# Kernel optimization log

Hardware: AMD Instinct MI355X
Metric: run time of the kernel (lower is better)

## Reference

```python
import jax, jax.numpy as jnp
import numpy as np

B, S, E, H = 4, 1024, 1024, 16
D = E // H  # head_dim = 64


def _rope_tables(seq_len, dim, base=10000.0):
    inv = 1.0 / (base ** (np.arange(0, dim, 2, dtype=np.float32) / dim))
    t = np.arange(seq_len, dtype=np.float32)
    freqs = np.outer(t, inv)                      # (S, D/2)
    emb = np.concatenate([freqs, freqs], axis=-1)  # (S, D)
    return (jnp.asarray(np.cos(emb))[None, None],  # (1,1,S,D)
            jnp.asarray(np.sin(emb))[None, None])


def setup_inputs() -> dict:
    key = jax.random.key(0)
    ks = jax.random.split(key, 12)
    std = 1.0 / np.sqrt(E)
    cos, sin = _rope_tables(S, D)
    # causal additive mask (2D, broadcast inside reference)
    neg = jnp.finfo(jnp.float32).min
    causal = jnp.where(jnp.tril(jnp.ones((S, S), dtype=bool)), 0.0, neg).astype(jnp.float32)
    return {
        "query": jax.random.normal(ks[0], (B, S, E), jnp.float32),
        "key": jax.random.normal(ks[1], (B, S, E), jnp.float32),
        "value": jax.random.normal(ks[2], (B, S, E), jnp.float32),
        "cos": cos,
        "sin": sin,
        "attn_mask": causal,
        "Wq": jax.random.uniform(ks[3], (E, E), jnp.float32, -std, std),
        "bq": jax.random.uniform(ks[4], (E,), jnp.float32, -std, std),
        "Wk": jax.random.uniform(ks[5], (E, E), jnp.float32, -std, std),
        "bk": jax.random.uniform(ks[6], (E,), jnp.float32, -std, std),
        "Wv": jax.random.uniform(ks[7], (E, E), jnp.float32, -std, std),
        "bv": jax.random.uniform(ks[8], (E,), jnp.float32, -std, std),
        "Wo": jax.random.uniform(ks[9], (E, E), jnp.float32, -std, std),
        "bo": jax.random.uniform(ks[10], (E,), jnp.float32, -std, std),
    }


def _rotate_half(x):
    x1, x2 = jnp.split(x, 2, axis=-1)
    return jnp.concatenate([-x2, x1], axis=-1)


def reference(query, key, value, cos, sin, attn_mask, Wq, bq, Wk, bk, Wv, bv, Wo, bo):
    b, sq, e = query.shape
    sk = key.shape[1]
    scale = D ** -0.5
    # projections (Linear stored as (in, out))
    q = (query @ Wq + bq).reshape(b, sq, H, D).transpose(0, 2, 1, 3)  # (B,H,Sq,D)
    k = (key @ Wk + bk).reshape(b, sk, H, D).transpose(0, 2, 1, 3)    # (B,H,Sk,D)
    v = (value @ Wv + bv).reshape(b, sk, H, D).transpose(0, 2, 1, 3)
    # rotary position embedding
    q = q * cos + _rotate_half(q) * sin
    k = k * cos + _rotate_half(k) * sin
    # scaled dot-product attention with additive mask
    scores = jnp.einsum("bhqd,bhkd->bhqk", q, k) * scale
    scores = scores + attn_mask[None, None]  # 2D mask -> broadcast over batch, heads
    attn = jax.nn.softmax(scores, axis=-1)
    out = jnp.einsum("bhqk,bhkd->bhqd", attn, v)
    out = out.transpose(0, 2, 1, 3).reshape(b, sq, e)
    return out @ Wo + bo
```

## Files before the change

kernel.cpp:

```cpp
#include <hip/hip_runtime.h>
#include <cmath>

#define S_LEN 1024
#define E_DIM 1024
#define NHEAD 16
#define HDIM  64
#define NBATCH 4
#define MROWS (NBATCH * S_LEN)

typedef unsigned short u16;
typedef unsigned long long u64;
typedef __bf16 bf16x8 __attribute__((ext_vector_type(8)));
typedef float  f32x4  __attribute__((ext_vector_type(4)));
typedef float  f4     __attribute__((ext_vector_type(4)));

union U64x2 { u64 u[2]; bf16x8 v; };

__device__ __forceinline__ float bf2f(u16 u) {
    union { unsigned int i; float f; } v; v.i = ((unsigned int)u) << 16; return v.f;
}
__device__ __forceinline__ u16 f2bf(float f) {
    union { float f; unsigned int i; } v; v.f = f;
    return (u16)((v.i + 0x7fffu + ((v.i >> 16) & 1u)) >> 16);
}
__device__ __forceinline__ int probe_f32(const void* cosT) {
    return ((const u16*)cosT)[0] != 0x3F80;
}
__device__ __forceinline__ void load16(u16* dst, const void* src, size_t eidx, int f32) {
    if (!f32) {
        const u16* p = (const u16*)src + eidx;
        *reinterpret_cast<int4*>(dst)     = *reinterpret_cast<const int4*>(p);
        *reinterpret_cast<int4*>(dst + 8) = *reinterpret_cast<const int4*>(p + 8);
    } else {
        const f4* p = reinterpret_cast<const f4*>((const float*)src + eidx);
        f4 a = p[0], b = p[1], c = p[2], d = p[3];
        dst[0]=f2bf(a.x);  dst[1]=f2bf(a.y);  dst[2]=f2bf(a.z);  dst[3]=f2bf(a.w);
        dst[4]=f2bf(b.x);  dst[5]=f2bf(b.y);  dst[6]=f2bf(b.z);  dst[7]=f2bf(b.w);
        dst[8]=f2bf(c.x);  dst[9]=f2bf(c.y);  dst[10]=f2bf(c.z); dst[11]=f2bf(c.w);
        dst[12]=f2bf(d.x); dst[13]=f2bf(d.y); dst[14]=f2bf(d.z); dst[15]=f2bf(d.w);
    }
}
__device__ __forceinline__ float ld1(const void* p, size_t i, int f32) {
    return f32 ? ((const float*)p)[i] : bf2f(((const u16*)p)[i]);
}
__device__ __forceinline__ void st1(void* p, size_t i, float v, int f32) {
    if (f32) ((float*)p)[i] = v; else ((u16*)p)[i] = f2bf(v);
}
__device__ __forceinline__ void gload16(const u16* gp, u16* lbase) {
    __builtin_amdgcn_global_load_lds(
        (const __attribute__((address_space(1))) void*)gp,
        (__attribute__((address_space(3))) void*)lbase, 16, 0, 0);
}

__global__ __launch_bounds__(256) void transpose_w(
    const void* __restrict__ W0, const void* __restrict__ W1,
    const void* __restrict__ W2, const void* __restrict__ W3,
    u16* __restrict__ T0, u16* __restrict__ T1,
    u16* __restrict__ T2, u16* __restrict__ T3,
    const void* __restrict__ cosT)
{
    __shared__ __align__(16) u16 tile[64][72];
    const int f32 = probe_f32(cosT);
    const int z = blockIdx.z;
    const void* W = (z == 0) ? W0 : (z == 1) ? W1 : (z == 2) ? W2 : W3;
    u16* T        = (z == 0) ? T0 : (z == 1) ? T1 : (z == 2) ? T2 : T3;
    const int r0 = blockIdx.y * 64, c0 = blockIdx.x * 64;
    const int tr = threadIdx.x >> 2, tc = (threadIdx.x & 3) * 16;

    load16(&tile[tr][tc], W, (size_t)(r0 + tr) * 1024 + c0 + tc, f32);
    __syncthreads();

    u16 buf[16];
#pragma unroll
    for (int j = 0; j < 16; ++j) buf[j] = tile[tc + j][tr];
    u16* dst = T + (size_t)(c0 + tr) * 1024 + r0 + tc;
    *reinterpret_cast<int4*>(dst)     = *reinterpret_cast<int4*>(buf);
    *reinterpret_cast<int4*>(dst + 8) = *reinterpret_cast<int4*>(buf + 8);
}

__device__ __forceinline__ void gemm_body64(
    const void* __restrict__ A, int aF, const u16* __restrict__ Wt,
    const void* __restrict__ bias, const void* __restrict__ cosT,
    const void* __restrict__ sinT, int tblF, void* __restrict__ C, int cF,
    int rope, float oscale, int m0, int n0)
{
    __shared__ __align__(16) u16 As[2][64 * 32];
    __shared__ __align__(16) u16 Bs[2][128 * 32];

    const int tid = threadIdx.x;
    const int w = tid >> 6, lane = tid & 63;
    const int lhi = lane >> 4, llo = lane & 15;
    const int jb0 = 4 * (w >> 1) + (w & 1);

    f32x4 acc[4][2];
#pragma unroll
    for (int i = 0; i < 4; ++i)
#pragma unroll
        for (int j = 0; j < 2; ++j) acc[i][j] = (f32x4){0.f, 0.f, 0.f, 0.f};

    const int srow = lane >> 2, spos = lane & 3;

    auto stage = [&](int buf, int k0) {
        if (!aF) {
            const int rowA = 16 * w + srow;
            const int cA = spos ^ ((rowA >> 1) & 3);
            gload16((const u16*)A + (size_t)(m0 + rowA) * 1024 + k0 + 8 * cA,
                    &As[buf][w * 512]);
        } else if (tid < 128) {
            const int row = tid >> 1, hc = tid & 1;
            u16 tmp[16];
            load16(tmp, A, (size_t)(m0 + row) * 1024 + k0 + 16 * hc, aF);
            const int g = (row >> 1) & 3;
            *reinterpret_cast<int4*>(&As[buf][row * 32 + ((2 * hc) ^ g) * 8]) =
                *reinterpret_cast<int4*>(tmp);
            *reinterpret_cast<int4*>(&As[buf][row * 32 + ((2 * hc + 1) ^ g) * 8]) =
                *reinterpret_cast<int4*>(tmp + 8);
        }
#pragma unroll
        for (int ss = 0; ss < 2; ++ss) {
            const int s = w + 4 * ss;
            const int row = 16 * s + srow;
            const int c = spos ^ ((row >> 1) & 3);
            gload16(Wt + (size_t)(n0 + row) * 1024 + k0 + 8 * c, &Bs[buf][s * 512]);
        }
    };

    auto compute = [&](int buf) {
        bf16x8 af[4], bfr[2];
#pragma unroll
        for (int mb = 0; mb < 4; ++mb) {
            const int r = 16 * mb + llo;
            af[mb] = *reinterpret_cast<const bf16x8*>(
                &As[buf][r * 32 + 8 * (lhi ^ ((r >> 1) & 3))]);
        }
#pragma unroll
        for (int j = 0; j < 2; ++j) {
            const int r = 16 * (jb0 + 2 * j) + llo;
            bfr[j] = *reinterpret_cast<const bf16x8*>(
                &Bs[buf][r * 32 + 8 * (lhi ^ ((r >> 1) & 3))]);
        }
#pragma unroll
        for (int mb = 0; mb < 4; ++mb)
#pragma unroll
            for (int j = 0; j < 2; ++j)
                acc[mb][j] = __builtin_amdgcn_mfma_f32_16x16x32_bf16(
                    af[mb], bfr[j], acc[mb][j], 0, 0, 0);
    };

    stage(0, 0);
    __syncthreads();
    int cur = 0;
    for (int k0 = 0; k0 < 1024; k0 += 32) {
        if (k0 + 32 < 1024) stage(cur ^ 1, k0 + 32);
        compute(cur);
        __syncthreads();
        cur ^= 1;
    }

    if (!rope) {
#pragma unroll
        for (int j = 0; j < 2; ++j) {
            const int colw = n0 + 16 * (jb0 + 2 * j) + llo;
            float bv = ld1(bias, colw, tblF);
#pragma unroll
            for (int mb = 0; mb < 4; ++mb) {
                int row = m0 + 16 * mb + 4 * lhi;
#pragma unroll
                for (int i = 0; i < 4; ++i)
                    st1(C, (size_t)(row + i) * 1024 + colw, acc[mb][j][i] + bv, cF);
            }
        }
    } else {
        const int d1 = 16 * (w & 1) + llo;
        const int c1 = n0 + 64 * (w >> 1) + d1;
        float b1 = ld1(bias, c1, tblF);
        float b2 = ld1(bias, c1 + 32, tblF);
#pragma unroll
        for (int mb = 0; mb < 4; ++mb) {
            int row = m0 + 16 * mb + 4 * lhi;
#pragma unroll
            for (int i = 0; i < 4; ++i) {
                int s = (row + i) & (S_LEN - 1);
                float c  = ld1(cosT, s * HDIM + d1, tblF);
                float sn = ld1(sinT, s * HDIM + d1, tblF);
                float x1 = acc[mb][0][i] + b1;
                float x2 = acc[mb][1][i] + b2;
                st1(C, (size_t)(row + i) * 1024 + c1,      (x1 * c - x2 * sn) * oscale, cF);
                st1(C, (size_t)(row + i) * 1024 + c1 + 32, (x2 * c + x1 * sn) * oscale, cF);
            }
        }
    }
}

__device__ __forceinline__ void gemm_body32(
    const void* __restrict__ A, int aF, const u16* __restrict__ Wt,
    const void* __restrict__ bias, const void* __restrict__ cosT,
    const void* __restrict__ sinT, int tblF, void* __restrict__ C, int cF,
    int rope, float oscale, int m0, int n0)
{
    __shared__ __align__(16) u16 As[2][32 * 32];
    __shared__ __align__(16) u16 Bs[2][128 * 32];

    const int tid = threadIdx.x;
    const int w = tid >> 6, lane = tid & 63;
    const int lhi = lane >> 4, llo = lane & 15;
    const int jb0 = 4 * (w >> 1) + (w & 1);

    f32x4 acc[2][2];
#pragma unroll
    for (int i = 0; i < 2; ++i)
#pragma unroll
        for (int j = 0; j < 2; ++j) acc[i][j] = (f32x4){0.f, 0.f, 0.f, 0.f};

    const int srow = lane >> 2, spos = lane & 3;

    auto stage = [&](int buf, int k0) {
        if (!aF) {
            if (w < 2) {
                const int rowA = 16 * w + srow;
                const int cA = spos ^ ((rowA >> 1) & 3);
                gload16((const u16*)A + (size_t)(m0 + rowA) * 1024 + k0 + 8 * cA,
                        &As[buf][w * 512]);
            }
        } else if (tid < 64) {
            const int row = tid >> 1, hc = tid & 1;
            u16 tmp[16];
            load16(tmp, A, (size_t)(m0 + row) * 1024 + k0 + 16 * hc, aF);
            const int g = (row >> 1) & 3;
            *reinterpret_cast<int4*>(&As[buf][row * 32 + ((2 * hc) ^ g) * 8]) =
                *reinterpret_cast<int4*>(tmp);
            *reinterpret_cast<int4*>(&As[buf][row * 32 + ((2 * hc + 1) ^ g) * 8]) =
                *reinterpret_cast<int4*>(tmp + 8);
        }
#pragma unroll
        for (int ss = 0; ss < 2; ++ss) {
            const int s = w + 4 * ss;
            const int row = 16 * s + srow;
            const int c = spos ^ ((row >> 1) & 3);
            gload16(Wt + (size_t)(n0 + row) * 1024 + k0 + 8 * c, &Bs[buf][s * 512]);
        }
    };

    auto compute = [&](int buf) {
        bf16x8 af[2], bfr[2];
#pragma unroll
        for (int mb = 0; mb < 2; ++mb) {
            const int r = 16 * mb + llo;
            af[mb] = *reinterpret_cast<const bf16x8*>(
                &As[buf][r * 32 + 8 * (lhi ^ ((r >> 1) & 3))]);
        }
#pragma unroll
        for (int j = 0; j < 2; ++j) {
            const int r = 16 * (jb0 + 2 * j) + llo;
            bfr[j] = *reinterpret_cast<const bf16x8*>(
                &Bs[buf][r * 32 + 8 * (lhi ^ ((r >> 1) & 3))]);
        }
#pragma unroll
        for (int mb = 0; mb < 2; ++mb)
#pragma unroll
            for (int j = 0; j < 2; ++j)
                acc[mb][j] = __builtin_amdgcn_mfma_f32_16x16x32_bf16(
                    af[mb], bfr[j], acc[mb][j], 0, 0, 0);
    };

    stage(0, 0);
    __syncthreads();
    int cur = 0;
    for (int k0 = 0; k0 < 1024; k0 += 32) {
        if (k0 + 32 < 1024) stage(cur ^ 1, k0 + 32);
        compute(cur);
        __syncthreads();
        cur ^= 1;
    }

    if (!rope) {
#pragma unroll
        for (int j = 0; j < 2; ++j) {
            const int colw = n0 + 16 * (jb0 + 2 * j) + llo;
            float bv = ld1(bias, colw, tblF);
#pragma unroll
            for (int mb = 0; mb < 2; ++mb) {
                int row = m0 + 16 * mb + 4 * lhi;
#pragma unroll
                for (int i = 0; i < 4; ++i)
                    st1(C, (size_t)(row + i) * 1024 + colw, acc[mb][j][i] + bv, cF);
            }
        }
    } else {
        const int d1 = 16 * (w & 1) + llo;
        const int c1 = n0 + 64 * (w >> 1) + d1;
        float b1 = ld1(bias, c1, tblF);
        float b2 = ld1(bias, c1 + 32, tblF);
#pragma unroll
        for (int mb = 0; mb < 2; ++mb) {
            int row = m0 + 16 * mb + 4 * lhi;
#pragma unroll
            for (int i = 0; i < 4; ++i) {
                int s = (row + i) & (S_LEN - 1);
                float c  = ld1(cosT, s * HDIM + d1, tblF);
                float sn = ld1(sinT, s * HDIM + d1, tblF);
                float x1 = acc[mb][0][i] + b1;
                float x2 = acc[mb][1][i] + b2;
                st1(C, (size_t)(row + i) * 1024 + c1,      (x1 * c - x2 * sn) * oscale, cF);
                st1(C, (size_t)(row + i) * 1024 + c1 + 32, (x2 * c + x1 * sn) * oscale, cF);
            }
        }
    }
}

__global__ __launch_bounds__(256, 6) void gemm_qkv(
    const void* __restrict__ q, const void* __restrict__ k, const void* __restrict__ v,
    const u16* __restrict__ WqT, const u16* __restrict__ WkT, const u16* __restrict__ WvT,
    const void* __restrict__ bq, const void* __restrict__ bk, const void* __restrict__ bv,
    const void* __restrict__ cosT, const void* __restrict__ sinT,
    u16* __restrict__ Qo, u16* __restrict__ Ko, u16* __restrict__ Vo)
{
    const int f32 = probe_f32(cosT);
    const int lin = blockIdx.x + 8 * (blockIdx.y + 64 * blockIdx.z);
    const int wg  = (lin & 7) * 192 + (lin >> 3);
    const int x = wg & 7, y = (wg >> 3) & 63, z = wg >> 9;
    const void* A  = (z == 0) ? q   : (z == 1) ? k   : v;
    const u16* Wt  = (z == 0) ? WqT : (z == 1) ? WkT : WvT;
    const void* b  = (z == 0) ? bq  : (z == 1) ? bk  : bv;
    u16* Co        = (z == 0) ? Qo  : (z == 1) ? Ko  : Vo;
    gemm_body64(A, f32, Wt, b, cosT, sinT, f32, Co, 0, (z < 2) ? 1 : 0,
                (z == 0) ? 0.125f : 1.0f, y * 64, x * 128);
}

__global__ __launch_bounds__(256, 8) void gemm_plain(
    const u16* __restrict__ Ain, const u16* __restrict__ Wt,
    const void* __restrict__ bias, const void* __restrict__ cosT,
    void* __restrict__ C)
{
    const int f32 = probe_f32(cosT);
    const int lin = blockIdx.x + 8 * blockIdx.y;
    const int wg  = (lin & 7) * 128 + (lin >> 3);
    const int x = wg & 7, y = wg >> 3;
    gemm_body32(Ain, 0, Wt, bias, nullptr, nullptr, f32, C, f32, 0, 1.0f,
                y * 32, x * 128);
}

__global__ __launch_bounds__(256, 4) void attn_fwd(
    const u16* __restrict__ Q, const u16* __restrict__ K,
    const u16* __restrict__ V, u16* __restrict__ O)
{
    __shared__ __align__(16) u16 Ks[2][64 * 64];
    __shared__ __align__(16) u16 Vt[64][68];
    __shared__ __align__(16) u16 Plds[4][16][68];

    const int tid = threadIdx.x;
    const int w = tid >> 6, lane = tid & 63;
    const int lhi = lane >> 4, llo = lane & 15;
    const int q0 = (int)(gridDim.x - 1 - blockIdx.x) * 64;
    const int bh = blockIdx.y;
    const int b = bh >> 4, h = bh & 15;
    const size_t base = (size_t)b * S_LEN * E_DIM + (size_t)h * HDIM;
    const u16* Qp = Q + base;
    const u16* Kp = K + base;
    const u16* Vp = V + base;
    const int wq0 = q0 + 16 * w;

    const int ksrow = lane >> 3, kpos = lane & 7;
    auto stageK = [&](int buf, int key0) {
#pragma unroll
        for (int ss = 0; ss < 2; ++ss) {
            const int s = w + 4 * ss;
            const int row = 8 * s + ksrow;
            const int c = kpos ^ (row & 7);
            gload16(Kp + (size_t)(key0 + row) * 1024 + 8 * c, &Ks[buf][s * 512]);
        }
    };
    const int vkey = tid & 63, vdc = tid >> 6;
    auto loadV = [&](int key0, int4* va, int4* vb) {
        const u16* vsrc = Vp + (size_t)(key0 + vkey) * 1024 + vdc * 16;
        *va = *reinterpret_cast<const int4*>(vsrc);
        *vb = *reinterpret_cast<const int4*>(vsrc + 8);
    };
    auto writeV = [&](int4 va, int4 vb) {
        u16 tmp[16];
        *reinterpret_cast<int4*>(tmp)     = va;
        *reinterpret_cast<int4*>(tmp + 8) = vb;
#pragma unroll
        for (int m = 0; m < 16; ++m) Vt[vdc * 16 + m][vkey] = tmp[m];
    };

    bf16x8 qf[2];
#pragma unroll
    for (int ds = 0; ds < 2; ++ds)
        qf[ds] = *reinterpret_cast<const bf16x8*>(
            Qp + (size_t)(wq0 + llo) * E_DIM + 32 * ds + 8 * lhi);

    f32x4 acco[4];
#pragma unroll
    for (int nb = 0; nb < 4; ++nb) acco[nb] = (f32x4){0.f, 0.f, 0.f, 0.f};
    float lrow[4] = {0.f, 0.f, 0.f, 0.f};

    stageK(0, 0);
    {
        int4 va, vb;
        loadV(0, &va, &vb);
        writeV(va, vb);
    }
    __syncthreads();

    const int dtiles = q0 >> 6;
    for (int t = 0; t <= dtiles; ++t) {
        const int cur = t & 1;
        const int key0 = t << 6;
        const bool nxt = (t < dtiles);

        int4 vva, vvb;
        if (nxt) {
            stageK(cur ^ 1, key0 + 64);
            loadV(key0 + 64, &vva, &vvb);
        }

        f32x4 sacc[4];
#pragma unroll
        for (int kb = 0; kb < 4; ++kb) sacc[kb] = (f32x4){0.f, 0.f, 0.f, 0.f};
        __builtin_amdgcn_s_setprio(1);
#pragma unroll
        for (int kb = 0; kb < 4; ++kb) {
            const int krow = 16 * kb + llo;
#pragma unroll
            for (int ds = 0; ds < 2; ++ds) {
                bf16x8 kf = *reinterpret_cast<const bf16x8*>(
                    &Ks[cur][krow * 64 + 8 * ((4 * ds + lhi) ^ (krow & 7))]);
                sacc[kb] = __builtin_amdgcn_mfma_f32_16x16x32_bf16(
                    qf[ds], kf, sacc[kb], 0, 0, 0);
            }
        }
        __builtin_amdgcn_s_setprio(0);

        const bool diag = (t == dtiles);
        float pv[4][4];
#pragma unroll
        for (int i = 0; i < 4; ++i) {
            const int qg = wq0 + 4 * lhi + i;
            float s0 = sacc[0][i];
            float s1 = sacc[1][i];
            float s2 = sacc[2][i];
            float s3 = sacc[3][i];
            if (diag) {
                if (key0 +      llo > qg) s0 = -3e38f;
                if (key0 + 16 + llo > qg) s1 = -3e38f;
                if (key0 + 32 + llo > qg) s2 = -3e38f;
                if (key0 + 48 + llo > qg) s3 = -3e38f;
            }
            float p0 = __expf(s0);
            float p1 = __expf(s1);
            float p2 = __expf(s2);
            float p3 = __expf(s3);
            lrow[i] += (p0 + p1) + (p2 + p3);
            pv[i][0] = p0; pv[i][1] = p1; pv[i][2] = p2; pv[i][3] = p3;
        }

#pragma unroll
        for (int kb = 0; kb < 4; ++kb)
#pragma unroll
            for (int i = 0; i < 4; ++i)
                Plds[w][4 * lhi + i][16 * kb + llo] = f2bf(pv[i][kb]);
        asm volatile("" ::: "memory");
        __builtin_amdgcn_sched_barrier(0);

        U64x2 pa[2];
#pragma unroll
        for (int ks = 0; ks < 2; ++ks) {
            const u16* pp = &Plds[w][llo][32 * ks + 8 * lhi];
            pa[ks].u[0] = *reinterpret_cast<const u64*>(pp);
            pa[ks].u[1] = *reinterpret_cast<const u64*>(pp + 4);
        }
        __builtin_amdgcn_s_setprio(1);
#pragma unroll
        for (int nb = 0; nb < 4; ++nb) {
#pragma unroll
            for (int ks = 0; ks < 2; ++ks) {
                const u16* vp = &Vt[16 * nb + llo][32 * ks + 8 * lhi];
                U64x2 vb;
                vb.u[0] = *reinterpret_cast<const u64*>(vp);
                vb.u[1] = *reinterpret_cast<const u64*>(vp + 4);
                acco[nb] = __builtin_amdgcn_mfma_f32_16x16x32_bf16(
                    pa[ks].v, vb.v, acco[nb], 0, 0, 0);
            }
        }
        __builtin_amdgcn_s_setprio(0);

        if (nxt) {
            __syncthreads();
            writeV(vva, vvb);
            __syncthreads();
        }
    }

    float linv[4];
#pragma unroll
    for (int i = 0; i < 4; ++i) {
        float rs = lrow[i];
#pragma unroll
        for (int off = 1; off < 16; off <<= 1) rs += __shfl_xor(rs, off, 64);
        linv[i] = 1.0f / rs;
    }
#pragma unroll
    for (int nb = 0; nb < 4; ++nb)
#pragma unroll
        for (int i = 0; i < 4; ++i) {
            int qg = wq0 + 4 * lhi + i;
            O[base + (size_t)qg * E_DIM + 16 * nb + llo] = f2bf(acco[nb][i] * linv[i]);
        }
}

extern "C" void kernel_launch(void* const* d_in, const int* in_sizes, int n_in,
                              void* d_out, int out_size, void* d_ws, size_t ws_size,
                              hipStream_t stream)
{
    const void* q    = d_in[0];
    const void* k    = d_in[1];
    const void* v    = d_in[2];
    const void* cosT = d_in[3];
    const void* sinT = d_in[4];
    const void* Wq   = d_in[6];
    const void* bq   = d_in[7];
    const void* Wk   = d_in[8];
    const void* bk   = d_in[9];
    const void* Wv   = d_in[10];
    const void* bv   = d_in[11];
    const void* Wo   = d_in[12];
    const void* bo   = d_in[13];

    const size_t mat = (size_t)MROWS * E_DIM;
    const size_t wsz = (size_t)E_DIM * E_DIM;
    u16* Qw  = (u16*)d_ws;
    u16* Kw  = Qw + mat;
    u16* Vw  = Kw + mat;
    u16* Ow  = Vw + mat;
    u16* WqT = Ow + mat;
    u16* WkT = WqT + wsz;
    u16* WvT = WkT + wsz;
    u16* WoT = WvT + wsz;

    transpose_w<<<dim3(16, 16, 4), 256, 0, stream>>>(Wq, Wk, Wv, Wo,
                                                     WqT, WkT, WvT, WoT, cosT);
    gemm_qkv<<<dim3(8, 64, 3), 256, 0, stream>>>(q, k, v, WqT, WkT, WvT,
                                                 bq, bk, bv, cosT, sinT, Qw, Kw, Vw);
    attn_fwd<<<dim3(16, 64), 256, 0, stream>>>(Qw, Kw, Vw, Ow);
    gemm_plain<<<dim3(8, 128), 256, 0, stream>>>(Ow, WoT, bo, cosT, (u16*)d_out);
}
```

Before: 124.5 us.

## Enlarge attention query tile to 128 rows with 8 waves sharing K/V tiles

```diff
diff --git a/kernel.cpp b/kernel.cpp
--- a/kernel.cpp
+++ b/kernel.cpp
@@ -340,18 +340,18 @@
                 y * 32, x * 128);
 }
 
-__global__ __launch_bounds__(256, 4) void attn_fwd(
+__global__ __launch_bounds__(512, 4) void attn_fwd(
     const u16* __restrict__ Q, const u16* __restrict__ K,
     const u16* __restrict__ V, u16* __restrict__ O)
 {
     __shared__ __align__(16) u16 Ks[2][64 * 64];
     __shared__ __align__(16) u16 Vt[64][68];
-    __shared__ __align__(16) u16 Plds[4][16][68];
+    __shared__ __align__(16) u16 Plds[8][16][68];
 
     const int tid = threadIdx.x;
     const int w = tid >> 6, lane = tid & 63;
     const int lhi = lane >> 4, llo = lane & 15;
-    const int q0 = (int)(gridDim.x - 1 - blockIdx.x) * 64;
+    const int q0 = (int)(gridDim.x - 1 - blockIdx.x) * 128;
     const int bh = blockIdx.y;
     const int b = bh >> 4, h = bh & 15;
     const size_t base = (size_t)b * S_LEN * E_DIM + (size_t)h * HDIM;
@@ -362,26 +362,20 @@
 
     const int ksrow = lane >> 3, kpos = lane & 7;
     auto stageK = [&](int buf, int key0) {
-#pragma unroll
-        for (int ss = 0; ss < 2; ++ss) {
-            const int s = w + 4 * ss;
-            const int row = 8 * s + ksrow;
-            const int c = kpos ^ (row & 7);
-            gload16(Kp + (size_t)(key0 + row) * 1024 + 8 * c, &Ks[buf][s * 512]);
-        }
+        const int row = 8 * w + ksrow;
+        const int c = kpos ^ (row & 7);
+        gload16(Kp + (size_t)(key0 + row) * 1024 + 8 * c, &Ks[buf][w * 512]);
     };
     const int vkey = tid & 63, vdc = tid >> 6;
-    auto loadV = [&](int key0, int4* va, int4* vb) {
-        const u16* vsrc = Vp + (size_t)(key0 + vkey) * 1024 + vdc * 16;
-        *va = *reinterpret_cast<const int4*>(vsrc);
-        *vb = *reinterpret_cast<const int4*>(vsrc + 8);
-    };
-    auto writeV = [&](int4 va, int4 vb) {
-        u16 tmp[16];
-        *reinterpret_cast<int4*>(tmp)     = va;
-        *reinterpret_cast<int4*>(tmp + 8) = vb;
-#pragma unroll
-        for (int m = 0; m < 16; ++m) Vt[vdc * 16 + m][vkey] = tmp[m];
+    auto loadV = [&](int key0, int4* va) {
+        *va = *reinterpret_cast<const int4*>(
+            Vp + (size_t)(key0 + vkey) * 1024 + vdc * 8);
+    };
+    auto writeV = [&](int4 va) {
+        u16 tmp[8];
+        *reinterpret_cast<int4*>(tmp) = va;
+#pragma unroll
+        for (int m = 0; m < 8; ++m) Vt[vdc * 8 + m][vkey] = tmp[m];
     };
 
     bf16x8 qf[2];
@@ -397,97 +391,101 @@
 
     stageK(0, 0);
     {
-        int4 va, vb;
-        loadV(0, &va, &vb);
-        writeV(va, vb);
+        int4 va;
+        loadV(0, &va);
+        writeV(va);
     }
     __syncthreads();
 
-    const int dtiles = q0 >> 6;
+    const int dtiles = (q0 >> 6) + 1;
     for (int t = 0; t <= dtiles; ++t) {
         const int cur = t & 1;
         const int key0 = t << 6;
         const bool nxt = (t < dtiles);
 
-        int4 vva, vvb;
+        int4 vva;
         if (nxt) {
             stageK(cur ^ 1, key0 + 64);
-            loadV(key0 + 64, &vva, &vvb);
-        }
-
-        f32x4 sacc[4];
-#pragma unroll
-        for (int kb = 0; kb < 4; ++kb) sacc[kb] = (f32x4){0.f, 0.f, 0.f, 0.f};
-        __builtin_amdgcn_s_setprio(1);
-#pragma unroll
-        for (int kb = 0; kb < 4; ++kb) {
-            const int krow = 16 * kb + llo;
-#pragma unroll
-            for (int ds = 0; ds < 2; ++ds) {
-                bf16x8 kf = *reinterpret_cast<const bf16x8*>(
-                    &Ks[cur][krow * 64 + 8 * ((4 * ds + lhi) ^ (krow & 7))]);
-                sacc[kb] = __builtin_amdgcn_mfma_f32_16x16x32_bf16(
-                    qf[ds], kf, sacc[kb], 0, 0, 0);
-            }
-        }
-        __builtin_amdgcn_s_setprio(0);
-
-        const bool diag = (t == dtiles);
-        float pv[4][4];
-#pragma unroll
-        for (int i = 0; i < 4; ++i) {
-            const int qg = wq0 + 4 * lhi + i;
-            float s0 = sacc[0][i];
-            float s1 = sacc[1][i];
-            float s2 = sacc[2][i];
-            float s3 = sacc[3][i];
-            if (diag) {
-                if (key0 +      llo > qg) s0 = -3e38f;
-                if (key0 + 16 + llo > qg) s1 = -3e38f;
-                if (key0 + 32 + llo > qg) s2 = -3e38f;
-                if (key0 + 48 + llo > qg) s3 = -3e38f;
-            }
-            float p0 = __expf(s0);
-            float p1 = __expf(s1);
-            float p2 = __expf(s2);
-            float p3 = __expf(s3);
-            lrow[i] += (p0 + p1) + (p2 + p3);
-            pv[i][0] = p0; pv[i][1] = p1; pv[i][2] = p2; pv[i][3] = p3;
-        }
-
-#pragma unroll
-        for (int kb = 0; kb < 4; ++kb)
-#pragma unroll
-            for (int i = 0; i < 4; ++i)
-                Plds[w][4 * lhi + i][16 * kb + llo] = f2bf(pv[i][kb]);
-        asm volatile("" ::: "memory");
-        __builtin_amdgcn_sched_barrier(0);
-
-        U64x2 pa[2];
-#pragma unroll
-        for (int ks = 0; ks < 2; ++ks) {
-            const u16* pp = &Plds[w][llo][32 * ks + 8 * lhi];
-            pa[ks].u[0] = *reinterpret_cast<const u64*>(pp);
-            pa[ks].u[1] = *reinterpret_cast<const u64*>(pp + 4);
-        }
-        __builtin_amdgcn_s_setprio(1);
-#pragma unroll
-        for (int nb = 0; nb < 4; ++nb) {
+            loadV(key0 + 64, &vva);
+        }
+
+        const bool active = (key0 <= wq0 + 15);
+        if (active) {
+            const bool needmask = (key0 + 63 > wq0);
+
+            f32x4 sacc[4];
+#pragma unroll
+            for (int kb = 0; kb < 4; ++kb) sacc[kb] = (f32x4){0.f, 0.f, 0.f, 0.f};
+            __builtin_amdgcn_s_setprio(1);
+#pragma unroll
+            for (int kb = 0; kb < 4; ++kb) {
+                const int krow = 16 * kb + llo;
+#pragma unroll
+                for (int ds = 0; ds < 2; ++ds) {
+                    bf16x8 kf = *reinterpret_cast<const bf16x8*>(
+                        &Ks[cur][krow * 64 + 8 * ((4 * ds + lhi) ^ (krow & 7))]);
+                    sacc[kb] = __builtin_amdgcn_mfma_f32_16x16x32_bf16(
+                        qf[ds], kf, sacc[kb], 0, 0, 0);
+                }
+            }
+            __builtin_amdgcn_s_setprio(0);
+
+            float pv[4][4];
+#pragma unroll
+            for (int i = 0; i < 4; ++i) {
+                const int qg = wq0 + 4 * lhi + i;
+                float s0 = sacc[0][i];
+                float s1 = sacc[1][i];
+                float s2 = sacc[2][i];
+                float s3 = sacc[3][i];
+                if (needmask) {
+                    if (key0 +      llo > qg) s0 = -3e38f;
+                    if (key0 + 16 + llo > qg) s1 = -3e38f;
+                    if (key0 + 32 + llo > qg) s2 = -3e38f;
+                    if (key0 + 48 + llo > qg) s3 = -3e38f;
+                }
+                float p0 = __expf(s0);
+                float p1 = __expf(s1);
+                float p2 = __expf(s2);
+                float p3 = __expf(s3);
+                lrow[i] += (p0 + p1) + (p2 + p3);
+                pv[i][0] = p0; pv[i][1] = p1; pv[i][2] = p2; pv[i][3] = p3;
+            }
+
+#pragma unroll
+            for (int kb = 0; kb < 4; ++kb)
+#pragma unroll
+                for (int i = 0; i < 4; ++i)
+                    Plds[w][4 * lhi + i][16 * kb + llo] = f2bf(pv[i][kb]);
+            asm volatile("" ::: "memory");
+            __builtin_amdgcn_sched_barrier(0);
+
+            U64x2 pa[2];
 #pragma unroll
             for (int ks = 0; ks < 2; ++ks) {
-                const u16* vp = &Vt[16 * nb + llo][32 * ks + 8 * lhi];
-                U64x2 vb;
-                vb.u[0] = *reinterpret_cast<const u64*>(vp);
-                vb.u[1] = *reinterpret_cast<const u64*>(vp + 4);
-                acco[nb] = __builtin_amdgcn_mfma_f32_16x16x32_bf16(
-                    pa[ks].v, vb.v, acco[nb], 0, 0, 0);
-            }
-        }
-        __builtin_amdgcn_s_setprio(0);
+                const u16* pp = &Plds[w][llo][32 * ks + 8 * lhi];
+                pa[ks].u[0] = *reinterpret_cast<const u64*>(pp);
+                pa[ks].u[1] = *reinterpret_cast<const u64*>(pp + 4);
+            }
+            __builtin_amdgcn_s_setprio(1);
+#pragma unroll
+            for (int nb = 0; nb < 4; ++nb) {
+#pragma unroll
+                for (int ks = 0; ks < 2; ++ks) {
+                    const u16* vp = &Vt[16 * nb + llo][32 * ks + 8 * lhi];
+                    U64x2 vb;
+                    vb.u[0] = *reinterpret_cast<const u64*>(vp);
+                    vb.u[1] = *reinterpret_cast<const u64*>(vp + 4);
+                    acco[nb] = __builtin_amdgcn_mfma_f32_16x16x32_bf16(
+                        pa[ks].v, vb.v, acco[nb], 0, 0, 0);
+                }
+            }
+            __builtin_amdgcn_s_setprio(0);
+        }
 
         if (nxt) {
             __syncthreads();
-            writeV(vva, vvb);
+            writeV(vva);
             __syncthreads();
         }
     }
@@ -542,6 +540,6 @@
                                                      WqT, WkT, WvT, WoT, cosT);
     gemm_qkv<<<dim3(8, 64, 3), 256, 0, stream>>>(q, k, v, WqT, WkT, WvT,
                                                  bq, bk, bv, cosT, sinT, Qw, Kw, Vw);
-    attn_fwd<<<dim3(16, 64), 256, 0, stream>>>(Qw, Kw, Vw, Ow);
+    attn_fwd<<<dim3(8, 64), 512, 0, stream>>>(Qw, Kw, Vw, Ow);
     gemm_plain<<<dim3(8, 128), 256, 0, stream>>>(Ow, WoT, bo, cosT, (u16*)d_out);
 }
```

Result: faster. 121.2 us (median of 2 runs) (-2.6%).
